# Kernel optimization log

Measured on AMD Instinct MI355X. Metric: run time of the kernel, lower is better.

The kernel has to match this reference:

```python
import jax, jax.numpy as jnp
import numpy as np

N_PTS = 100000
N_VERTS = 6890
N_JOINTS = 24


def build_rotation(q):
    # q: [N,4] unnormalized quaternions (w, x, y, z) -> [N,3,3] rotation matrices
    q = q / jnp.linalg.norm(q, axis=-1, keepdims=True)
    r, x, y, z = q[:, 0], q[:, 1], q[:, 2], q[:, 3]
    R = jnp.stack([
        1 - 2 * (y * y + z * z), 2 * (x * y - r * z), 2 * (x * z + r * y),
        2 * (x * y + r * z), 1 - 2 * (x * x + z * z), 2 * (y * z - r * x),
        2 * (x * z - r * y), 2 * (y * z + r * x), 1 - 2 * (x * x + y * y),
    ], axis=-1)
    return R.reshape(-1, 3, 3)


def setup_inputs() -> dict:
    key = jax.random.key(0)
    k1, k2, k3, k4, k5 = jax.random.split(key, 5)
    xyz = jax.random.normal(k1, (N_PTS, 3), dtype=jnp.float32)
    rotation = jax.random.normal(k2, (N_PTS, 4), dtype=jnp.float32)
    smpl_verts = jax.random.normal(k3, (N_VERTS, 3), dtype=jnp.float32)
    sw = jax.random.uniform(k4, (N_VERTS, N_JOINTS), dtype=jnp.float32)
    skinning_weights = sw / jnp.sum(sw, axis=-1, keepdims=True)  # rows sum to 1, like LBS weights
    transforms_mat = jax.random.normal(k5, (N_JOINTS, 4, 4), dtype=jnp.float32)
    return {"xyz": xyz, "rotation": rotation, "smpl_verts": smpl_verts,
            "skinning_weights": skinning_weights, "transforms_mat": transforms_mat}


def reference(xyz, rotation, smpl_verts, skinning_weights, transforms_mat):
    n_pts = xyz.shape[0]
    # --- brute-force 1-NN (knn_points, K=1) via squared Euclidean distance ---
    # d2[n, v] = |x_n|^2 - 2 x_n . v + |v|^2  -> [N, 6890]
    d2 = (jnp.sum(xyz * xyz, axis=-1, keepdims=True)
          - 2.0 * (xyz @ smpl_verts.T)
          + jnp.sum(smpl_verts * smpl_verts, axis=-1)[None, :])
    p_idx = jnp.argmin(d2, axis=-1)  # [N]
    # --- gather per-point skinning weights ---
    pts_W = skinning_weights[p_idx, :]  # [N, 24]
    # --- blend joint transforms: (N,24) @ (24,16) -> (N,4,4) ---
    T_fwd = (pts_W @ transforms_mat.reshape(-1, 16)).reshape(n_pts, 4, 4)
    # --- transform points homogeneously ---
    x_homo = jnp.concatenate([xyz, jnp.ones((n_pts, 1), dtype=xyz.dtype)], axis=-1)  # [N,4]
    x_bar = jnp.einsum('nij,nj->ni', T_fwd, x_homo)[:, :3]  # [N,3]
    # --- rotate gaussian orientations ---
    rotation_hat = build_rotation(rotation)  # [N,3,3]
    rotation_bar = jnp.einsum('nij,njk->nik', T_fwd[:, :3, :3], rotation_hat)  # [N,3,3]
    return x_bar, rotation_bar, T_fwd
```

## Files before the change

kernel.cpp:

```cpp
#include <hip/hip_runtime.h>
#include <math.h>

#define NPTS 100000
#define NVERTS 6890
#define NJ 24

#define NTILE 216
#define CPT 24
#define NCHK 9
#define TILE_F4 96
#define CHUNK_F4 (CPT * TILE_F4)
#define REC_F4 (NCHK * CHUNK_F4)

typedef short bf16x8 __attribute__((ext_vector_type(8)));
typedef float f32x16 __attribute__((ext_vector_type(16)));

__device__ __forceinline__ unsigned short bf16_rtne(float f) {
    const unsigned int u = __float_as_uint(f);
    return (unsigned short)((u + 0x7FFFu + ((u >> 16) & 1u)) >> 16);
}
__device__ __forceinline__ float bf16_back(unsigned short h) {
    return __uint_as_float(((unsigned int)h) << 16);
}
__device__ __forceinline__ float min16(const f32x16 a) {
    float t0 = fminf(a[0], a[1]),  t1 = fminf(a[2], a[3]);
    float t2 = fminf(a[4], a[5]),  t3 = fminf(a[6], a[7]);
    float t4 = fminf(a[8], a[9]),  t5 = fminf(a[10], a[11]);
    float t6 = fminf(a[12], a[13]), t7 = fminf(a[14], a[15]);
    t0 = fminf(t0, t1); t2 = fminf(t2, t3); t4 = fminf(t4, t5); t6 = fminf(t6, t7);
    return fminf(fminf(t0, t2), fminf(t4, t6));
}

__global__ void prep_kernel(const float* __restrict__ verts, float4* __restrict__ recG)
{
#pragma clang fp contract(off)
    const int v = blockIdx.x * 256 + threadIdx.x;
    if (v >= NTILE * 32) return;
    const int t_glob = v >> 5, row = v & 31;
    float4* base = recG + (t_glob / CPT) * CHUNK_F4 + (t_glob % CPT) * TILE_F4;

    float cx = 0.f, cy = 0.f, cz = 0.f, vsq;
    unsigned short vh0, vh1, vh2, vl0, vl1, vl2, qh, ql;
    const short one = (short)0x3F80;
    if (v < NVERTS) {
        cx = verts[v * 3 + 0]; cy = verts[v * 3 + 1]; cz = verts[v * 3 + 2];
        vsq = (cx * cx + cy * cy) + cz * cz;
        vh0 = bf16_rtne(cx); vl0 = bf16_rtne(cx - bf16_back(vh0));
        vh1 = bf16_rtne(cy); vl1 = bf16_rtne(cy - bf16_back(vh1));
        vh2 = bf16_rtne(cz); vl2 = bf16_rtne(cz - bf16_back(vh2));
        qh = bf16_rtne(vsq); ql = bf16_rtne(vsq - bf16_back(qh));
    } else {
        vh0 = vh1 = vh2 = vl0 = vl1 = vl2 = 0;
        qh = bf16_rtne(30000.0f); ql = 0; vsq = 1e30f;
    }
    union { bf16x8 s; float4 f; } r0, r1;
    r0.s = (bf16x8){(short)vh0, (short)vh1, (short)vh2,
                    (short)vl0, (short)vl1, (short)vl2, (short)vh0, (short)vh1};
    r1.s = (bf16x8){(short)vh2, (short)qh, (short)ql, one, one, 0, 0, 0};
    base[row]      = r0.f;
    base[32 + row] = r1.f;
    base[64 + row] = make_float4(cx, cy, cz, vsq);
}

__global__ __launch_bounds__(256) void nn_mfma_kernel(
    const float* __restrict__ xyz,
    const float4* __restrict__ recG,
    unsigned long long* __restrict__ best_ws)
{
#pragma clang fp contract(off)
    __shared__ float4 smem[CHUNK_F4];
    const int tid = threadIdx.x;
    const int lane = tid & 63;
    const int wid = tid >> 6;
    const int half = lane >> 5;
    const int col = lane & 31;

    const int p = blockIdx.x * 128 + wid * 32 + col;
    const int pe = (p < NPTS) ? p : (NPTS - 1);
    const float x = xyz[pe * 3 + 0], y = xyz[pe * 3 + 1], z = xyz[pe * 3 + 2];
    const float xsq = (x * x + y * y) + z * z;

    const float ux = -2.0f * x, uy = -2.0f * y, uz = -2.0f * z;
    const unsigned short uh0 = bf16_rtne(ux), uh1 = bf16_rtne(uy), uh2 = bf16_rtne(uz);
    const unsigned short ul0 = bf16_rtne(ux - bf16_back(uh0));
    const unsigned short ul1 = bf16_rtne(uy - bf16_back(uh1));
    const unsigned short ul2 = bf16_rtne(uz - bf16_back(uh2));
    const unsigned short qh = bf16_rtne(xsq);
    const unsigned short ql = bf16_rtne(xsq - bf16_back(qh));
    const short one = (short)0x3F80;
    bf16x8 bfrag;
    if (half == 0)
        bfrag = (bf16x8){(short)uh0, (short)uh1, (short)uh2,
                         (short)uh0, (short)uh1, (short)uh2, (short)ul0, (short)ul1};
    else
        bfrag = (bf16x8){(short)ul2, one, one, (short)qh, (short)ql, 0, 0, 0};

    const f32x16 zacc = {0.f};
    const int aidx = half * 32 + col;

    float run = 1e30f;
    for (int c = 0; c < NCHK; ++c) {
        __syncthreads();
        const float4* src = recG + c * CHUNK_F4;
        for (int i = tid; i < CHUNK_F4; i += 256) smem[i] = src[i];
        __syncthreads();
        for (int t = 0; t < CPT; ++t) {
            union { float4 f; bf16x8 s; } a;
            a.f = smem[t * TILE_F4 + aidx];
            const f32x16 acc = __builtin_amdgcn_mfma_f32_32x32x16_bf16(a.s, bfrag, zacc, 0, 0, 0);
            run = fminf(run, min16(acc));
        }
    }
    const float m = fminf(run, __shfl_xor(run, 32));
    const float thr = m + (1.5e-4f + 1.5e-4f * xsq + 1.0e-4f * m);

    for (int c = 0; c < NCHK; ++c) {
        __syncthreads();
        const float4* src = recG + c * CHUNK_F4;
        for (int i = tid; i < CHUNK_F4; i += 256) smem[i] = src[i];
        __syncthreads();
        for (int t = 0; t < CPT; ++t) {
            union { float4 f; bf16x8 s; } a;
            a.f = smem[t * TILE_F4 + aidx];
            const f32x16 acc = __builtin_amdgcn_mfma_f32_32x32x16_bf16(a.s, bfrag, zacc, 0, 0, 0);
            if (min16(acc) <= thr) {
                #pragma unroll
                for (int e = 0; e < 16; ++e) {
                    if (acc[e] <= thr) {
                        const int row = (e & 3) + 8 * (e >> 2) + 4 * half;
                        const float4 vr = smem[t * TILE_F4 + 64 + row];
                        float g = x * vr.x;
                        g = fmaf(y, vr.y, g);
                        g = fmaf(z, vr.z, g);
                        const float tt = fmaf(-2.0f, g, xsq);
                        const float d2 = tt + vr.w;
                        const int vg = c * (CPT * 32) + t * 32 + row;
                        const unsigned long long pk =
                            ((unsigned long long)__float_as_uint(d2) << 32) | (unsigned)vg;
                        atomicMin(&best_ws[pe], pk);
                    }
                }
            }
        }
    }
}

__global__ __launch_bounds__(256) void apply_kernel(
    const float* __restrict__ xyz,
    const float* __restrict__ rot,
    const float* __restrict__ sw,
    const float* __restrict__ tm,
    const unsigned long long* __restrict__ best_ws,
    float* __restrict__ out)
{
    __shared__ float tl[NJ * 16];
    const int tid = threadIdx.x;
    for (int i = tid; i < NJ * 16; i += 256) tl[i] = tm[i];
    __syncthreads();

    const int p = blockIdx.x * 256 + tid;
    if (p >= NPTS) return;

    const int vi = (int)(best_ws[p] & 0xFFFFFFFFull);
    const float4* w4 = reinterpret_cast<const float4*>(sw + (size_t)vi * NJ);

    float T[16];
    #pragma unroll
    for (int i = 0; i < 16; ++i) T[i] = 0.0f;

    #pragma unroll
    for (int jq = 0; jq < NJ / 4; ++jq) {
        const float4 wv = w4[jq];
        const float wj[4] = { wv.x, wv.y, wv.z, wv.w };
        #pragma unroll
        for (int k = 0; k < 4; ++k) {
            const int j = jq * 4 + k;
            #pragma unroll
            for (int i = 0; i < 16; ++i)
                T[i] = fmaf(wj[k], tl[j * 16 + i], T[i]);
        }
    }

    const float4 q = reinterpret_cast<const float4*>(rot)[p];
    float qr = q.x, qx = q.y, qy = q.z, qz = q.w;
    const float inv = 1.0f / sqrtf(qr * qr + qx * qx + qy * qy + qz * qz);
    qr *= inv; qx *= inv; qy *= inv; qz *= inv;
    float R[9];
    R[0] = 1.0f - 2.0f * (qy * qy + qz * qz);
    R[1] = 2.0f * (qx * qy - qr * qz);
    R[2] = 2.0f * (qx * qz + qr * qy);
    R[3] = 2.0f * (qx * qy + qr * qz);
    R[4] = 1.0f - 2.0f * (qx * qx + qz * qz);
    R[5] = 2.0f * (qy * qz - qr * qx);
    R[6] = 2.0f * (qx * qz - qr * qy);
    R[7] = 2.0f * (qy * qz + qr * qx);
    R[8] = 1.0f - 2.0f * (qx * qx + qy * qy);

    const float x0 = xyz[p * 3 + 0];
    const float x1 = xyz[p * 3 + 1];
    const float x2 = xyz[p * 3 + 2];

    #pragma unroll
    for (int i = 0; i < 3; ++i) {
        out[p * 3 + i] = fmaf(T[i * 4 + 0], x0,
                          fmaf(T[i * 4 + 1], x1,
                           fmaf(T[i * 4 + 2], x2, T[i * 4 + 3])));
    }

    float* rb = out + 300000 + (size_t)p * 9;
    #pragma unroll
    for (int i = 0; i < 3; ++i) {
        #pragma unroll
        for (int k = 0; k < 3; ++k) {
            rb[i * 3 + k] = fmaf(T[i * 4 + 0], R[0 * 3 + k],
                             fmaf(T[i * 4 + 1], R[1 * 3 + k],
                                  T[i * 4 + 2] * R[2 * 3 + k]));
        }
    }

    float* tb = out + 1200000 + (size_t)p * 16;
    #pragma unroll
    for (int i = 0; i < 16; ++i) tb[i] = T[i];
}

extern "C" void kernel_launch(void* const* d_in, const int* in_sizes, int n_in,
                              void* d_out, int out_size, void* d_ws, size_t ws_size,
                              hipStream_t stream) {
    const float* xyz   = (const float*)d_in[0];
    const float* rot   = (const float*)d_in[1];
    const float* verts = (const float*)d_in[2];
    const float* sw    = (const float*)d_in[3];
    const float* tm    = (const float*)d_in[4];
    float* out = (float*)d_out;

    unsigned long long* best_ws = (unsigned long long*)d_ws;
    float4* recG = (float4*)((char*)d_ws + (1 << 20));

    hipMemsetAsync(d_ws, 0xFF, NPTS * sizeof(unsigned long long), stream);

    prep_kernel<<<(NTILE * 32 + 255) / 256, 256, 0, stream>>>(verts, recG);
    nn_mfma_kernel<<<(NPTS + 127) / 128, 256, 0, stream>>>(xyz, recG, best_ws);
    apply_kernel<<<(NPTS + 255) / 256, 256, 0, stream>>>(xyz, rot, sw, tm, best_ws, out);
}
```

Baseline: 161.1 us.

## Read vertex tiles directly from global memory and use v_min3 reductions

Removes the LDS staging of vertex chunks and the __syncthreads barriers around each chunk. Every wave now loads its MFMA A-fragment and the fp32 vertex records straight from global memory, relying on L1/L2 caching, with the tile loop unrolled by two. The min16 reduction is rewritten with inline v_min3_f32 to cut the number of min instructions. The trade-off is higher global and cache load latency per tile in place of cheap LDS reads, with no barrier to hide it.

```diff
diff --git a/kernel.cpp b/kernel.cpp
--- a/kernel.cpp
+++ b/kernel.cpp
@@ -6,11 +6,7 @@
 #define NJ 24
 
 #define NTILE 216
-#define CPT 24
-#define NCHK 9
 #define TILE_F4 96
-#define CHUNK_F4 (CPT * TILE_F4)
-#define REC_F4 (NCHK * CHUNK_F4)
 
 typedef short bf16x8 __attribute__((ext_vector_type(8)));
 typedef float f32x16 __attribute__((ext_vector_type(16)));
@@ -22,13 +18,20 @@
 __device__ __forceinline__ float bf16_back(unsigned short h) {
     return __uint_as_float(((unsigned int)h) << 16);
 }
+__device__ __forceinline__ float min3f(float a, float b, float c) {
+    float d;
+    asm("v_min3_f32 %0, %1, %2, %3" : "=v"(d) : "v"(a), "v"(b), "v"(c));
+    return d;
+}
 __device__ __forceinline__ float min16(const f32x16 a) {
-    float t0 = fminf(a[0], a[1]),  t1 = fminf(a[2], a[3]);
-    float t2 = fminf(a[4], a[5]),  t3 = fminf(a[6], a[7]);
-    float t4 = fminf(a[8], a[9]),  t5 = fminf(a[10], a[11]);
-    float t6 = fminf(a[12], a[13]), t7 = fminf(a[14], a[15]);
-    t0 = fminf(t0, t1); t2 = fminf(t2, t3); t4 = fminf(t4, t5); t6 = fminf(t6, t7);
-    return fminf(fminf(t0, t2), fminf(t4, t6));
+    const float m0 = min3f(a[0], a[1], a[2]);
+    const float m1 = min3f(a[3], a[4], a[5]);
+    const float m2 = min3f(a[6], a[7], a[8]);
+    const float m3 = min3f(a[9], a[10], a[11]);
+    const float m4 = min3f(a[12], a[13], a[14]);
+    const float n0 = min3f(m0, m1, m2);
+    const float n1 = min3f(m3, m4, a[15]);
+    return fminf(n0, n1);
 }
 
 __global__ void prep_kernel(const float* __restrict__ verts, float4* __restrict__ recG)
@@ -37,7 +40,7 @@
     const int v = blockIdx.x * 256 + threadIdx.x;
     if (v >= NTILE * 32) return;
     const int t_glob = v >> 5, row = v & 31;
-    float4* base = recG + (t_glob / CPT) * CHUNK_F4 + (t_glob % CPT) * TILE_F4;
+    float4* base = recG + t_glob * TILE_F4;
 
     float cx = 0.f, cy = 0.f, cz = 0.f, vsq;
     unsigned short vh0, vh1, vh2, vl0, vl1, vl2, qh, ql;
@@ -68,7 +71,6 @@
     unsigned long long* __restrict__ best_ws)
 {
 #pragma clang fp contract(off)
-    __shared__ float4 smem[CHUNK_F4];
     const int tid = threadIdx.x;
     const int lane = tid & 63;
     const int wid = tid >> 6;
@@ -96,49 +98,39 @@
         bfrag = (bf16x8){(short)ul2, one, one, (short)qh, (short)ql, 0, 0, 0};
 
     const f32x16 zacc = {0.f};
-    const int aidx = half * 32 + col;
+    const int aoff = half * 32 + col;
 
     float run = 1e30f;
-    for (int c = 0; c < NCHK; ++c) {
-        __syncthreads();
-        const float4* src = recG + c * CHUNK_F4;
-        for (int i = tid; i < CHUNK_F4; i += 256) smem[i] = src[i];
-        __syncthreads();
-        for (int t = 0; t < CPT; ++t) {
-            union { float4 f; bf16x8 s; } a;
-            a.f = smem[t * TILE_F4 + aidx];
-            const f32x16 acc = __builtin_amdgcn_mfma_f32_32x32x16_bf16(a.s, bfrag, zacc, 0, 0, 0);
-            run = fminf(run, min16(acc));
-        }
+    #pragma unroll 2
+    for (int t = 0; t < NTILE; ++t) {
+        union { float4 f; bf16x8 s; } a;
+        a.f = recG[t * TILE_F4 + aoff];
+        const f32x16 acc = __builtin_amdgcn_mfma_f32_32x32x16_bf16(a.s, bfrag, zacc, 0, 0, 0);
+        run = fminf(run, min16(acc));
     }
     const float m = fminf(run, __shfl_xor(run, 32));
     const float thr = m + (1.5e-4f + 1.5e-4f * xsq + 1.0e-4f * m);
 
-    for (int c = 0; c < NCHK; ++c) {
-        __syncthreads();
-        const float4* src = recG + c * CHUNK_F4;
-        for (int i = tid; i < CHUNK_F4; i += 256) smem[i] = src[i];
-        __syncthreads();
-        for (int t = 0; t < CPT; ++t) {
-            union { float4 f; bf16x8 s; } a;
-            a.f = smem[t * TILE_F4 + aidx];
-            const f32x16 acc = __builtin_amdgcn_mfma_f32_32x32x16_bf16(a.s, bfrag, zacc, 0, 0, 0);
-            if (min16(acc) <= thr) {
-                #pragma unroll
-                for (int e = 0; e < 16; ++e) {
-                    if (acc[e] <= thr) {
-                        const int row = (e & 3) + 8 * (e >> 2) + 4 * half;
-                        const float4 vr = smem[t * TILE_F4 + 64 + row];
-                        float g = x * vr.x;
-                        g = fmaf(y, vr.y, g);
-                        g = fmaf(z, vr.z, g);
-                        const float tt = fmaf(-2.0f, g, xsq);
-                        const float d2 = tt + vr.w;
-                        const int vg = c * (CPT * 32) + t * 32 + row;
-                        const unsigned long long pk =
-                            ((unsigned long long)__float_as_uint(d2) << 32) | (unsigned)vg;
-                        atomicMin(&best_ws[pe], pk);
-                    }
+    #pragma unroll 2
+    for (int t = 0; t < NTILE; ++t) {
+        union { float4 f; bf16x8 s; } a;
+        a.f = recG[t * TILE_F4 + aoff];
+        const f32x16 acc = __builtin_amdgcn_mfma_f32_32x32x16_bf16(a.s, bfrag, zacc, 0, 0, 0);
+        if (min16(acc) <= thr) {
+            #pragma unroll
+            for (int e = 0; e < 16; ++e) {
+                if (acc[e] <= thr) {
+                    const int row = (e & 3) + 8 * (e >> 2) + 4 * half;
+                    const float4 vr = recG[t * TILE_F4 + 64 + row];
+                    float g = x * vr.x;
+                    g = fmaf(y, vr.y, g);
+                    g = fmaf(z, vr.z, g);
+                    const float tt = fmaf(-2.0f, g, xsq);
+                    const float d2 = tt + vr.w;
+                    const int vg = t * 32 + row;
+                    const unsigned long long pk =
+                        ((unsigned long long)__float_as_uint(d2) << 32) | (unsigned)vg;
+                    atomicMin(&best_ws[pe], pk);
                 }
             }
         }
```

After: 168.9 us. 4.9% more time.
